# Performance work log

Measured on AMD Instinct MI355X. Metric: run time of the kernel, lower is better.

The kernel has to match this reference:

```python
import jax, jax.numpy as jnp
import numpy as np

NUM_HEADS = 8
NUM_POINTS = 4


def setup_inputs() -> dict:
    key = jax.random.key(0)
    ks = jax.random.split(key, 8)
    B, N, C, H, W = 8, 8192, 256, 128, 128
    HP2 = NUM_HEADS * NUM_POINTS * 2
    HP = NUM_HEADS * NUM_POINTS
    query = jax.random.normal(ks[0], (B, N, C), jnp.float32)
    reference_points = jax.random.uniform(ks[1], (B, N, 2), dtype=jnp.float32)
    value = jax.random.normal(ks[2], (B, C, H, W), jnp.float32)
    # learned params (offset gen is zero-init in the original; use small random
    W_off = jax.random.normal(ks[3], (C, HP2), jnp.float32) * 0.02
    b_off = jnp.zeros((HP2,), jnp.float32)
    W_attn = jax.random.normal(ks[4], (C, HP), jnp.float32) * (1.0 / np.sqrt(C))
    b_attn = jnp.zeros((HP,), jnp.float32)
    W_out = jax.random.normal(ks[5], (C, C), jnp.float32) * (1.0 / np.sqrt(C))
    b_out = jnp.zeros((C,), jnp.float32)
    return dict(query=query, reference_points=reference_points, value=value,
                W_off=W_off, b_off=b_off, W_attn=W_attn, b_attn=b_attn,
                W_out=W_out, b_out=b_out, H=H, W=W)


def reference(query, reference_points, value, W_off, b_off, W_attn, b_attn,
              W_out, b_out, H, W):
    B, N, C = query.shape
    Hh, P = NUM_HEADS, NUM_POINTS
    D = C // Hh

    offset = (query @ W_off + b_off).reshape(B, N, Hh, P, 2)
    attn = jax.nn.softmax((query @ W_attn + b_attn).reshape(B, N, Hh, P), axis=-1)

    # sampling locations in grid_sample convention: (x, y) in [-1, 1]
    ref = reference_points * 2.0 - 1.0
    loc = ref[:, :, None, None, :] + offset  # (B, N, Hh, P, 2)

    # value -> (B, Hh, H*W, D)
    val = value.reshape(B, Hh, D, H, W).transpose(0, 1, 3, 4, 2).reshape(B, Hh, H * W, D)

    # align_corners=False pixel coordinates
    x = (loc[..., 0] + 1.0) * (W * 0.5) - 0.5  # (B, N, Hh, P)
    y = (loc[..., 1] + 1.0) * (H * 0.5) - 0.5
    x0f = jnp.floor(x); y0f = jnp.floor(y)
    wx1 = x - x0f; wy1 = y - y0f
    x0 = x0f.astype(jnp.int32); y0 = y0f.astype(jnp.int32)
    x1 = x0 + 1; y1 = y0 + 1

    def gather(ix, iy, w):
        # bilinear corner gather with zero padding (mask out-of-bounds)
        valid = (ix >= 0) & (ix < W) & (iy >= 0) & (iy < H)
        idx = jnp.clip(iy, 0, H - 1) * W + jnp.clip(ix, 0, W - 1)  # (B,N,Hh,P)
        idx_t = idx.transpose(0, 2, 1, 3).reshape(B, Hh, N * P)
        g = jnp.take_along_axis(val, idx_t[..., None], axis=2)  # (B,Hh,N*P,D)
        g = g.reshape(B, Hh, N, P, D).transpose(0, 2, 1, 3, 4)  # (B,N,Hh,P,D)
        return g * (w * valid)[..., None]

    sampled = (gather(x0, y0, (1 - wx1) * (1 - wy1))
               + gather(x1, y0, wx1 * (1 - wy1))
               + gather(x0, y1, (1 - wx1) * wy1)
               + gather(x1, y1, wx1 * wy1))  # (B,N,Hh,P,D)

    out = jnp.einsum('bnhk,bnhkd->bnhd', attn, sampled).reshape(B, N, C)
    return out @ W_out + b_out
```

## Files before the change

### kernel.cpp

```cpp
#include <hip/hip_runtime.h>
#include <hip/hip_bf16.h>
#include <cstddef>

#define B_  8
#define N_  8192
#define C_  256
#define H_  128
#define W_  128
#define HH  8
#define PP  4
#define DD  32
#define HW  (H_ * W_)

typedef short bf16x8 __attribute__((ext_vector_type(8)));
typedef float f32x4  __attribute__((ext_vector_type(4)));

static __device__ __forceinline__ short f2bf_s(float f) {
    __hip_bfloat16 b = __float2bfloat16(f);
    return *reinterpret_cast<short*>(&b);
}
static __device__ __forceinline__ float bf_s2f(short s) {
    __hip_bfloat16 b = *reinterpret_cast<__hip_bfloat16*>(&s);
    return __bfloat162float(b);
}

__global__ __launch_bounds__(256) void kTP(const float* __restrict__ value,
                                           __hip_bfloat16* __restrict__ val,
                                           const float* __restrict__ W_off,
                                           const float* __restrict__ W_attn,
                                           short* __restrict__ Wc_hi,
                                           short* __restrict__ Wc_lo,
                                           const float* __restrict__ Wsrc,
                                           __hip_bfloat16* __restrict__ Wt) {
    __shared__ __align__(16) char smem[33024];
    const int t   = threadIdx.x;
    const int bid = blockIdx.x;

    if (bid < 4096) {
        float (*tile)[257] = (float (*)[257])smem;
        const int bh   = bid >> 6;
        const int pix0 = (bid & 63) * 256;
        const float* src = value + (size_t)bh * 32 * HW + pix0;
#pragma unroll
        for (int i = 0; i < 8; ++i) {
            int d  = i * 4 + (t >> 6);
            int p4 = t & 63;
            float4 v = *(const float4*)&src[(size_t)d * HW + p4 * 4];
            tile[d][p4 * 4 + 0] = v.x;
            tile[d][p4 * 4 + 1] = v.y;
            tile[d][p4 * 4 + 2] = v.z;
            tile[d][p4 * 4 + 3] = v.w;
        }
        __syncthreads();
#pragma unroll
        for (int j = 0; j < 4; ++j) {
            int pix = j * 64 + (t >> 2);
            int d0  = (t & 3) * 8;
            bf16x8 o;
#pragma unroll
            for (int k = 0; k < 8; ++k) o[k] = f2bf_s(tile[d0 + k][pix]);
            *(bf16x8*)&val[((size_t)bh * HW + pix0 + pix) * 32 + d0] = o;
        }
    } else if (bid < 4192) {
        const int c = bid - 4096;
        float v = (c < 64) ? W_off[(size_t)t * 64 + c]
                           : W_attn[(size_t)t * 32 + (c - 64)];
        short h = f2bf_s(v);
        short l = f2bf_s(v - bf_s2f(h));
        Wc_hi[(size_t)c * 256 + t] = h;
        Wc_lo[(size_t)c * 256 + t] = l;
    } else {
        float (*tile)[65] = (float (*)[65])smem;
        const int bx = bid - 4192;
        const int n0 = (bx & 3) * 64;
        const int k0 = (bx >> 2) * 64;
#pragma unroll
        for (int i = 0; i < 16; ++i) {
            int kk = i * 4 + (t >> 6);
            int nn = t & 63;
            tile[kk][nn] = Wsrc[(size_t)(k0 + kk) * 256 + n0 + nn];
        }
        __syncthreads();
#pragma unroll
        for (int i = 0; i < 16; ++i) {
            int nn = i * 4 + (t >> 6);
            int kk = t & 63;
            Wt[(size_t)(n0 + nn) * 256 + k0 + kk] = __float2bfloat16(tile[kk][nn]);
        }
    }
}

__global__ __launch_bounds__(256) void kA1M(const float* __restrict__ query,
                                            const float* __restrict__ refp,
                                            const short* __restrict__ Wc_hi,
                                            const short* __restrict__ Wc_lo,
                                            const float* __restrict__ b_off,
                                            const float* __restrict__ b_attn,
                                            float4* __restrict__ locattn) {
    __shared__ __align__(16) char smem[57344];
    short* As_hi = (short*)smem;
    short* As_lo = (short*)(smem + 16384);
    short* Bs_hi = (short*)(smem + 32768);
    short* Bs_lo = (short*)(smem + 45056);
    float* Ct    = (float*)smem;

    const int t    = threadIdx.x;
    const int lane = t & 63;
    const int w    = t >> 6;
    const int wm   = (w & 1) * 64;
    const int wn   = (w >> 1) * 48;
    const int quad = lane >> 4;
    const int l16  = lane & 15;
    const int row0 = blockIdx.x * 128;

    f32x4 acc[4][3];
#pragma unroll
    for (int mt = 0; mt < 4; ++mt)
#pragma unroll
        for (int nt = 0; nt < 3; ++nt)
            acc[mt][nt] = (f32x4){0.f, 0.f, 0.f, 0.f};

    for (int k0c = 0; k0c < 4; ++k0c) {
#pragma unroll
        for (int i = 0; i < 8; ++i) {
            int f   = t + i * 256;
            int row = f >> 4;
            int kq4 = f & 15;
            float4 q = *(const float4*)&query[(size_t)(row0 + row) * 256 +
                                              k0c * 64 + kq4 * 4];
            short4 hv, lv;
            hv.x = f2bf_s(q.x); lv.x = f2bf_s(q.x - bf_s2f(hv.x));
            hv.y = f2bf_s(q.y); lv.y = f2bf_s(q.y - bf_s2f(hv.y));
            hv.z = f2bf_s(q.z); lv.z = f2bf_s(q.z - bf_s2f(hv.z));
            hv.w = f2bf_s(q.w); lv.w = f2bf_s(q.w - bf_s2f(hv.w));
            int base = row * 64 + (((kq4 >> 1) ^ (row & 7)) * 8) + (kq4 & 1) * 4;
            *(short4*)&As_hi[base] = hv;
            *(short4*)&As_lo[base] = lv;
        }
#pragma unroll
        for (int i = 0; i < 3; ++i) {
            int idx = t + i * 256;
            int n   = idx >> 3;
            int kb  = idx & 7;
            int dst = n * 64 + ((kb ^ (n & 7)) * 8);
            *(uint4*)&Bs_hi[dst] =
                *(const uint4*)&Wc_hi[(size_t)n * 256 + k0c * 64 + kb * 8];
            *(uint4*)&Bs_lo[dst] =
                *(const uint4*)&Wc_lo[(size_t)n * 256 + k0c * 64 + kb * 8];
        }
        __syncthreads();

#pragma unroll
        for (int ks = 0; ks < 2; ++ks) {
            const int kq = ks * 4 + quad;
            bf16x8 ah[4], al[4], bh[3], bl[3];
#pragma unroll
            for (int mt = 0; mt < 4; ++mt) {
                int m = wm + mt * 16 + l16;
                ah[mt] = *(const bf16x8*)&As_hi[m * 64 + (kq ^ (m & 7)) * 8];
                al[mt] = *(const bf16x8*)&As_lo[m * 64 + (kq ^ (m & 7)) * 8];
            }
#pragma unroll
            for (int nt = 0; nt < 3; ++nt) {
                int n = wn + nt * 16 + l16;
                bh[nt] = *(const bf16x8*)&Bs_hi[n * 64 + (kq ^ (n & 7)) * 8];
                bl[nt] = *(const bf16x8*)&Bs_lo[n * 64 + (kq ^ (n & 7)) * 8];
            }
#pragma unroll
            for (int mt = 0; mt < 4; ++mt)
#pragma unroll
                for (int nt = 0; nt < 3; ++nt)
                    acc[mt][nt] = __builtin_amdgcn_mfma_f32_16x16x32_bf16(
                        ah[mt], bh[nt], acc[mt][nt], 0, 0, 0);
#pragma unroll
            for (int mt = 0; mt < 4; ++mt)
#pragma unroll
                for (int nt = 0; nt < 3; ++nt)
                    acc[mt][nt] = __builtin_amdgcn_mfma_f32_16x16x32_bf16(
                        ah[mt], bl[nt], acc[mt][nt], 0, 0, 0);
#pragma unroll
            for (int mt = 0; mt < 4; ++mt)
#pragma unroll
                for (int nt = 0; nt < 3; ++nt)
                    acc[mt][nt] = __builtin_amdgcn_mfma_f32_16x16x32_bf16(
                        al[mt], bh[nt], acc[mt][nt], 0, 0, 0);
        }
        __syncthreads();
    }

#pragma unroll
    for (int mt = 0; mt < 4; ++mt) {
#pragma unroll
        for (int nt = 0; nt < 3; ++nt) {
            int col = wn + nt * 16 + l16;
#pragma unroll
            for (int rI = 0; rI < 4; ++rI) {
                int row = wm + mt * 16 + quad * 4 + rI;
                Ct[row * 100 + col] = acc[mt][nt][rI];
            }
        }
    }
    __syncthreads();

    const int rg = t >> 3;
    const int h  = t & 7;
    float boff[8];
#pragma unroll
    for (int j = 0; j < 8; ++j) boff[j] = b_off[h * 8 + j];
    float batn[4];
#pragma unroll
    for (int j = 0; j < 4; ++j) batn[j] = b_attn[h * 4 + j];

#pragma unroll
    for (int r = 0; r < 4; ++r) {
        int row  = rg * 4 + r;
        int rowg = row0 + row;
        float rx = refp[(size_t)rowg * 2 + 0];
        float ry = refp[(size_t)rowg * 2 + 1];
        float4 lg4 = *(const float4*)&Ct[row * 100 + 64 + h * 4];
        float lg[4] = {lg4.x + batn[0], lg4.y + batn[1],
                       lg4.z + batn[2], lg4.w + batn[3]};
        float m = fmaxf(fmaxf(lg[0], lg[1]), fmaxf(lg[2], lg[3]));
        float e[4];
        float s = 0.f;
#pragma unroll
        for (int p = 0; p < 4; ++p) { e[p] = __expf(lg[p] - m); s += e[p]; }
        float inv = 1.f / s;
        float4 o0 = *(const float4*)&Ct[row * 100 + h * 8];
        float4 o1 = *(const float4*)&Ct[row * 100 + h * 8 + 4];
        float ox[4] = {o0.x + boff[0], o0.z + boff[2],
                       o1.x + boff[4], o1.z + boff[6]};
        float oy[4] = {o0.y + boff[1], o0.w + boff[3],
                       o1.y + boff[5], o1.w + boff[7]};
#pragma unroll
        for (int p = 0; p < 4; ++p) {
            float x = (rx * 2.f + ox[p]) * (W_ * 0.5f) - 0.5f;
            float y = (ry * 2.f + oy[p]) * (H_ * 0.5f) - 0.5f;
            locattn[(size_t)rowg * 32 + h * 4 + p] =
                make_float4(x, y, e[p] * inv, 0.f);
        }
    }
}

__global__ __launch_bounds__(256) void kA2(const float4* __restrict__ locattn,
                                           const __hip_bfloat16* __restrict__ val,
                                           __hip_bfloat16* __restrict__ mid) {
    __shared__ float2 ow[64][4][4];

    const int t   = threadIdx.x;
    const int bid = blockIdx.x;
    const int xcd = bid & 7;
    const int j_  = bid >> 3;
    const int bh  = xcd * 8 + (j_ >> 7);
    const int n0  = (j_ & 127) * 64;
    const int b   = bh >> 3;
    const int h   = bh & 7;

    {
        const int r = t >> 2;
        const int p = t & 3;
        float4 L = locattn[((size_t)b * N_ + n0 + r) * 32 + h * 4 + p];
        float x = L.x, y = L.y, a = L.z;
        float xf = floorf(x), yf = floorf(y);
        int x0 = (int)xf, y0 = (int)yf;
        int x1 = x0 + 1, y1 = y0 + 1;
        float wx1 = x - xf, wy1 = y - yf;
        float wx0 = 1.f - wx1, wy0 = 1.f - wy1;
        int cx0 = min(max(x0, 0), W_ - 1);
        int cx1 = min(max(x1, 0), W_ - 1);
        int cy0 = min(max(y0, 0), H_ - 1);
        int cy1 = min(max(y1, 0), H_ - 1);
        bool bx0 = (x0 >= 0) & (x0 < W_);
        bool bx1 = (x1 >= 0) & (x1 < W_);
        bool by0 = (y0 >= 0) & (y0 < H_);
        bool by1 = (y1 >= 0) & (y1 < H_);
        float w00 = a * wx0 * wy0 * ((bx0 & by0) ? 1.f : 0.f);
        float w10 = a * wx1 * wy0 * ((bx1 & by0) ? 1.f : 0.f);
        float w01 = a * wx0 * wy1 * ((bx0 & by1) ? 1.f : 0.f);
        float w11 = a * wx1 * wy1 * ((bx1 & by1) ? 1.f : 0.f);
        ow[r][p][0] = make_float2(__int_as_float(cy0 * W_ + cx0), w00);
        ow[r][p][1] = make_float2(__int_as_float(cy0 * W_ + cx1), w10);
        ow[r][p][2] = make_float2(__int_as_float(cy1 * W_ + cx0), w01);
        ow[r][p][3] = make_float2(__int_as_float(cy1 * W_ + cx1), w11);
    }
    __syncthreads();

    const int d  = t & 31;
    const int rg = t >> 5;
    const __hip_bfloat16* vb = val + (size_t)bh * HW * DD + d;
    __hip_bfloat16* mo = mid + ((size_t)b * N_ + n0) * C_ + h * DD + d;

#pragma unroll
    for (int j = 0; j < 8; ++j) {
        int r = rg * 8 + j;
        const float4* owp = (const float4*)&ow[r][0][0];
        float acc = 0.f;
#pragma unroll
        for (int p = 0; p < 4; ++p) {
            float4 u0 = owp[p * 2 + 0];
            float4 u1 = owp[p * 2 + 1];
            int o00 = __float_as_int(u0.x) * DD;
            int o10 = __float_as_int(u0.z) * DD;
            int o01 = __float_as_int(u1.x) * DD;
            int o11 = __float_as_int(u1.z) * DD;
            acc += u0.y * __bfloat162float(vb[o00]);
            acc += u0.w * __bfloat162float(vb[o10]);
            acc += u1.y * __bfloat162float(vb[o01]);
            acc += u1.w * __bfloat162float(vb[o11]);
        }
        mo[r * C_] = __float2bfloat16(acc);
    }
}

__global__ __launch_bounds__(256) void kC(const short* __restrict__ mid,
                                          const short* __restrict__ Wt,
                                          const float* __restrict__ bias,
                                          float* __restrict__ out) {
    __shared__ __align__(16) short As[128 * 64];
    __shared__ __align__(16) short Bs[128 * 64];

    const int t    = threadIdx.x;
    const int lane = t & 63;
    const int w    = t >> 6;
    const int wm   = (w & 1) * 64;
    const int wn   = (w >> 1) * 64;
    const int row0 = blockIdx.x * 128;
    const int col0 = blockIdx.y * 128;

    f32x4 acc[4][4];
#pragma unroll
    for (int mt = 0; mt < 4; ++mt)
#pragma unroll
        for (int nt = 0; nt < 4; ++nt)
            acc[mt][nt] = (f32x4){0.f, 0.f, 0.f, 0.f};

    const int sr = t >> 3;
    const int kb = t & 7;

    for (int k0 = 0; k0 < 4; ++k0) {
#pragma unroll
        for (int i = 0; i < 4; ++i) {
            int row  = sr + i * 32;
            int kbs  = (kb ^ (row & 7)) * 8;
            *(uint4*)&As[row * 64 + kbs] =
                *(const uint4*)&mid[(size_t)(row0 + row) * 256 + k0 * 64 + kb * 8];
            *(uint4*)&Bs[row * 64 + kbs] =
                *(const uint4*)&Wt[(size_t)(col0 + row) * 256 + k0 * 64 + kb * 8];
        }
        __syncthreads();

#pragma unroll
        for (int ks = 0; ks < 2; ++ks) {
            const int kq = ks * 4 + (lane >> 4);
            bf16x8 af[4], bf[4];
#pragma unroll
            for (int mt = 0; mt < 4; ++mt) {
                int m = wm + mt * 16 + (lane & 15);
                af[mt] = *(const bf16x8*)&As[m * 64 + (kq ^ (m & 7)) * 8];
            }
#pragma unroll
            for (int nt = 0; nt < 4; ++nt) {
                int n = wn + nt * 16 + (lane & 15);
                bf[nt] = *(const bf16x8*)&Bs[n * 64 + (kq ^ (n & 7)) * 8];
            }
#pragma unroll
            for (int mt = 0; mt < 4; ++mt)
#pragma unroll
                for (int nt = 0; nt < 4; ++nt)
                    acc[mt][nt] = __builtin_amdgcn_mfma_f32_16x16x32_bf16(
                        af[mt], bf[nt], acc[mt][nt], 0, 0, 0);
        }
        __syncthreads();
    }

    const int cq = lane >> 4;
#pragma unroll
    for (int nt = 0; nt < 4; ++nt) {
        int col  = col0 + wn + nt * 16 + (lane & 15);
        float bv = bias[col];
#pragma unroll
        for (int mt = 0; mt < 4; ++mt) {
#pragma unroll
            for (int rI = 0; rI < 4; ++rI) {
                int rowg = row0 + wm + mt * 16 + cq * 4 + rI;
                out[(size_t)rowg * 256 + col] = acc[mt][nt][rI] + bv;
            }
        }
    }
}

extern "C" void kernel_launch(void* const* d_in, const int* in_sizes, int n_in,
                              void* d_out, int out_size, void* d_ws, size_t ws_size,
                              hipStream_t stream) {
    const float* query  = (const float*)d_in[0];
    const float* refp   = (const float*)d_in[1];
    const float* value  = (const float*)d_in[2];
    const float* W_off  = (const float*)d_in[3];
    const float* b_off  = (const float*)d_in[4];
    const float* W_attn = (const float*)d_in[5];
    const float* b_attn = (const float*)d_in[6];
    const float* W_out  = (const float*)d_in[7];
    const float* b_out  = (const float*)d_in[8];
    float* out = (float*)d_out;

    char*           ws      = (char*)d_ws;
    __hip_bfloat16* val     = (__hip_bfloat16*)(ws);
    float4*         locattn = (float4*)(ws + 67108864);
    __hip_bfloat16* mid     = (__hip_bfloat16*)(ws + 100663296);
    __hip_bfloat16* Wt      = (__hip_bfloat16*)(ws + 134217728);
    short*          Wc_hi   = (short*)(ws + 134348800);
    short*          Wc_lo   = (short*)(ws + 134397952);

    kTP <<<dim3(4208), 256, 0, stream>>>(value, val, W_off, W_attn,
                                         Wc_hi, Wc_lo, W_out, Wt);
    kA1M<<<dim3((B_ * N_) / 128), 256, 0, stream>>>(query, refp, Wc_hi, Wc_lo,
                                                    b_off, b_attn, locattn);
    kA2 <<<dim3(B_ * HH * N_ / 64), 256, 0, stream>>>(locattn, val, mid);
    kC  <<<dim3((B_ * N_) / 128, C_ / 128), 256, 0, stream>>>(
        (const short*)mid, (const short*)Wt, b_out, out);
}
```

Before: 381.6 us.

## Fuse bilinear sampling with output projection GEMM using fp16 packed math

Merges the sampling kernel and the output-projection GEMM into one kernel. Each block builds a 64-row by 256-channel intermediate in shared memory and multiplies it by W_out with MFMA, so the mid buffer never makes a global write and read round trip. The value tensor and W_out move from bf16 to fp16, and sampling uses packed half2 FMAs with 4-channel vector gathers and compressed index/weight records. W_out tiles are register-prefetched one k-step ahead. The cost is lower accumulation precision (fp16 sums), and with 64-row blocks W_out is reloaded for every block.

```diff
diff --git a/kernel.cpp b/kernel.cpp
--- a/kernel.cpp
+++ b/kernel.cpp
@@ -1,5 +1,6 @@
 #include <hip/hip_runtime.h>
 #include <hip/hip_bf16.h>
+#include <hip/hip_fp16.h>
 #include <cstddef>
 
 #define B_  8
@@ -13,6 +14,7 @@
 #define HW  (H_ * W_)
 
 typedef short bf16x8 __attribute__((ext_vector_type(8)));
+typedef _Float16 f16x8 __attribute__((ext_vector_type(8)));
 typedef float f32x4  __attribute__((ext_vector_type(4)));
 
 static __device__ __forceinline__ short f2bf_s(float f) {
@@ -25,13 +27,13 @@
 }
 
 __global__ __launch_bounds__(256) void kTP(const float* __restrict__ value,
-                                           __hip_bfloat16* __restrict__ val,
+                                           __half* __restrict__ val,
                                            const float* __restrict__ W_off,
                                            const float* __restrict__ W_attn,
                                            short* __restrict__ Wc_hi,
                                            short* __restrict__ Wc_lo,
                                            const float* __restrict__ Wsrc,
-                                           __hip_bfloat16* __restrict__ Wt) {
+                                           __half* __restrict__ Wt) {
     __shared__ __align__(16) char smem[33024];
     const int t   = threadIdx.x;
     const int bid = blockIdx.x;
@@ -56,10 +58,14 @@
         for (int j = 0; j < 4; ++j) {
             int pix = j * 64 + (t >> 2);
             int d0  = (t & 3) * 8;
-            bf16x8 o;
-#pragma unroll
-            for (int k = 0; k < 8; ++k) o[k] = f2bf_s(tile[d0 + k][pix]);
-            *(bf16x8*)&val[((size_t)bh * HW + pix0 + pix) * 32 + d0] = o;
+            short o[8];
+#pragma unroll
+            for (int k = 0; k < 8; ++k) {
+                __half hh = __float2half(tile[d0 + k][pix]);
+                o[k] = *reinterpret_cast<short*>(&hh);
+            }
+            *(bf16x8*)&val[((size_t)bh * HW + pix0 + pix) * 32 + d0] =
+                *(bf16x8*)o;
         }
     } else if (bid < 4192) {
         const int c = bid - 4096;
@@ -85,7 +91,7 @@
         for (int i = 0; i < 16; ++i) {
             int nn = i * 4 + (t >> 6);
             int kk = t & 63;
-            Wt[(size_t)(n0 + nn) * 256 + k0 + kk] = __float2bfloat16(tile[kk][nn]);
+            Wt[(size_t)(n0 + nn) * 256 + k0 + kk] = __float2half(tile[kk][nn]);
         }
     }
 }
@@ -242,24 +248,36 @@
     }
 }
 
-__global__ __launch_bounds__(256) void kA2(const float4* __restrict__ locattn,
-                                           const __hip_bfloat16* __restrict__ val,
-                                           __hip_bfloat16* __restrict__ mid) {
-    __shared__ float2 ow[64][4][4];
-
-    const int t   = threadIdx.x;
-    const int bid = blockIdx.x;
-    const int xcd = bid & 7;
-    const int j_  = bid >> 3;
-    const int bh  = xcd * 8 + (j_ >> 7);
-    const int n0  = (j_ & 127) * 64;
-    const int b   = bh >> 3;
-    const int h   = bh & 7;
-
-    {
-        const int r = t >> 2;
-        const int p = t & 3;
-        float4 L = locattn[((size_t)b * N_ + n0 + r) * 32 + h * 4 + p];
+__global__ __launch_bounds__(256) void kAC(const float4* __restrict__ locattn,
+                                           const __half* __restrict__ val,
+                                           const __half* __restrict__ Wt,
+                                           const float* __restrict__ bias,
+                                           float* __restrict__ out) {
+    __shared__ __align__(16) char smem[65536];
+    char*  midc = smem;
+    uint4* ow   = (uint4*)(smem + 32768);
+    short* Bs   = (short*)(smem + 32768);
+
+    const int t    = threadIdx.x;
+    const int bid  = blockIdx.x;
+    const int b    = bid & 7;
+    const int n0   = (bid >> 3) * 64;
+
+    const int pn  = t >> 3;
+    const int pkb = t & 7;
+    uint4 pre[8];
+#pragma unroll
+    for (int i = 0; i < 8; ++i) {
+        int n = pn + i * 32;
+        pre[i] = *(const uint4*)&Wt[(size_t)n * 256 + pkb * 8];
+    }
+
+#pragma unroll
+    for (int i = 0; i < 8; ++i) {
+        int item = t + i * 256;
+        int r  = item >> 5;
+        int hp = item & 31;
+        float4 L = locattn[((size_t)b * N_ + n0 + r) * 32 + hp];
         float x = L.x, y = L.y, a = L.z;
         float xf = floorf(x), yf = floorf(y);
         int x0 = (int)xf, y0 = (int)yf;
@@ -274,58 +292,73 @@
         bool bx1 = (x1 >= 0) & (x1 < W_);
         bool by0 = (y0 >= 0) & (y0 < H_);
         bool by1 = (y1 >= 0) & (y1 < H_);
-        float w00 = a * wx0 * wy0 * ((bx0 & by0) ? 1.f : 0.f);
-        float w10 = a * wx1 * wy0 * ((bx1 & by0) ? 1.f : 0.f);
-        float w01 = a * wx0 * wy1 * ((bx0 & by1) ? 1.f : 0.f);
-        float w11 = a * wx1 * wy1 * ((bx1 & by1) ? 1.f : 0.f);
-        ow[r][p][0] = make_float2(__int_as_float(cy0 * W_ + cx0), w00);
-        ow[r][p][1] = make_float2(__int_as_float(cy0 * W_ + cx1), w10);
-        ow[r][p][2] = make_float2(__int_as_float(cy1 * W_ + cx0), w01);
-        ow[r][p][3] = make_float2(__int_as_float(cy1 * W_ + cx1), w11);
+        float f00 = a * wx0 * wy0 * ((bx0 & by0) ? 1.f : 0.f);
+        float f10 = a * wx1 * wy0 * ((bx1 & by0) ? 1.f : 0.f);
+        float f01 = a * wx0 * wy1 * ((bx0 & by1) ? 1.f : 0.f);
+        float f11 = a * wx1 * wy1 * ((bx1 & by1) ? 1.f : 0.f);
+        uint4 rec;
+        rec.x = (unsigned)(cy0 * W_ + cx0) | ((unsigned)(cy0 * W_ + cx1) << 16);
+        rec.y = (unsigned)(cy1 * W_ + cx0) | ((unsigned)(cy1 * W_ + cx1) << 16);
+        __half2 wA = __floats2half2_rn(f00, f10);
+        __half2 wB = __floats2half2_rn(f01, f11);
+        rec.z = *reinterpret_cast<unsigned*>(&wA);
+        rec.w = *reinterpret_cast<unsigned*>(&wB);
+        ow[item] = rec;
     }
     __syncthreads();
 
-    const int d  = t & 31;
-    const int rg = t >> 5;
-    const __hip_bfloat16* vb = val + (size_t)bh * HW * DD + d;
-    __hip_bfloat16* mo = mid + ((size_t)b * N_ + n0) * C_ + h * DD + d;
-
-#pragma unroll
-    for (int j = 0; j < 8; ++j) {
-        int r = rg * 8 + j;
-        const float4* owp = (const float4*)&ow[r][0][0];
-        float acc = 0.f;
-#pragma unroll
-        for (int p = 0; p < 4; ++p) {
-            float4 u0 = owp[p * 2 + 0];
-            float4 u1 = owp[p * 2 + 1];
-            int o00 = __float_as_int(u0.x) * DD;
-            int o10 = __float_as_int(u0.z) * DD;
-            int o01 = __float_as_int(u1.x) * DD;
-            int o11 = __float_as_int(u1.z) * DD;
-            acc += u0.y * __bfloat162float(vb[o00]);
-            acc += u0.w * __bfloat162float(vb[o10]);
-            acc += u1.y * __bfloat162float(vb[o01]);
-            acc += u1.w * __bfloat162float(vb[o11]);
-        }
-        mo[r * C_] = __float2bfloat16(acc);
-    }
-}
-
-__global__ __launch_bounds__(256) void kC(const short* __restrict__ mid,
-                                          const short* __restrict__ Wt,
-                                          const float* __restrict__ bias,
-                                          float* __restrict__ out) {
-    __shared__ __align__(16) short As[128 * 64];
-    __shared__ __align__(16) short Bs[128 * 64];
-
-    const int t    = threadIdx.x;
+    {
+        const int j8 = t & 7;
+        const int g  = t >> 3;
+        const int d8 = j8 * 4;
+#pragma unroll
+        for (int q = 0; q < 16; ++q) {
+            int pair = g * 16 + q;
+            int r = pair >> 3;
+            int h = pair & 7;
+            const char* vb = (const char*)val +
+                ((((size_t)b * 8 + h) * HW) * 32 + d8) * 2;
+            __half2 a01 = __float2half2_rn(0.f);
+            __half2 a23 = __float2half2_rn(0.f);
+#pragma unroll
+            for (int p = 0; p < 4; ++p) {
+                uint4 rec = ow[r * 32 + h * 4 + p];
+                int i0 = rec.x & 0xffff, i1 = rec.x >> 16;
+                int i2 = rec.y & 0xffff, i3 = rec.y >> 16;
+                __half2 wA = *reinterpret_cast<__half2*>(&rec.z);
+                __half2 wB = *reinterpret_cast<__half2*>(&rec.w);
+                uint2 u0 = *(const uint2*)(vb + (size_t)i0 * 64);
+                uint2 u1 = *(const uint2*)(vb + (size_t)i1 * 64);
+                uint2 u2 = *(const uint2*)(vb + (size_t)i2 * 64);
+                uint2 u3 = *(const uint2*)(vb + (size_t)i3 * 64);
+                __half2 w00 = __low2half2(wA);
+                a01 = __hfma2(*reinterpret_cast<__half2*>(&u0.x), w00, a01);
+                a23 = __hfma2(*reinterpret_cast<__half2*>(&u0.y), w00, a23);
+                __half2 w10 = __high2half2(wA);
+                a01 = __hfma2(*reinterpret_cast<__half2*>(&u1.x), w10, a01);
+                a23 = __hfma2(*reinterpret_cast<__half2*>(&u1.y), w10, a23);
+                __half2 w01 = __low2half2(wB);
+                a01 = __hfma2(*reinterpret_cast<__half2*>(&u2.x), w01, a01);
+                a23 = __hfma2(*reinterpret_cast<__half2*>(&u2.y), w01, a23);
+                __half2 w11 = __high2half2(wB);
+                a01 = __hfma2(*reinterpret_cast<__half2*>(&u3.x), w11, a01);
+                a23 = __hfma2(*reinterpret_cast<__half2*>(&u3.y), w11, a23);
+            }
+            int c8  = h * 4 + (d8 >> 3);
+            int off = r * 512 + ((c8 ^ (r & 7)) * 16) + (d8 & 7) * 2;
+            uint2 st;
+            st.x = *reinterpret_cast<unsigned*>(&a01);
+            st.y = *reinterpret_cast<unsigned*>(&a23);
+            *(uint2*)(midc + off) = st;
+        }
+    }
+    __syncthreads();
+
     const int lane = t & 63;
     const int w    = t >> 6;
-    const int wm   = (w & 1) * 64;
-    const int wn   = (w >> 1) * 64;
-    const int row0 = blockIdx.x * 128;
-    const int col0 = blockIdx.y * 128;
+    const int wn   = w * 64;
+    const int quad = lane >> 4;
+    const int l16  = lane & 15;
 
     f32x4 acc[4][4];
 #pragma unroll
@@ -334,56 +367,58 @@
         for (int nt = 0; nt < 4; ++nt)
             acc[mt][nt] = (f32x4){0.f, 0.f, 0.f, 0.f};
 
-    const int sr = t >> 3;
-    const int kb = t & 7;
-
     for (int k0 = 0; k0 < 4; ++k0) {
 #pragma unroll
-        for (int i = 0; i < 4; ++i) {
-            int row  = sr + i * 32;
-            int kbs  = (kb ^ (row & 7)) * 8;
-            *(uint4*)&As[row * 64 + kbs] =
-                *(const uint4*)&mid[(size_t)(row0 + row) * 256 + k0 * 64 + kb * 8];
-            *(uint4*)&Bs[row * 64 + kbs] =
-                *(const uint4*)&Wt[(size_t)(col0 + row) * 256 + k0 * 64 + kb * 8];
+        for (int i = 0; i < 8; ++i) {
+            int n = pn + i * 32;
+            *(uint4*)&Bs[n * 64 + ((pkb ^ (n & 7)) * 8)] = pre[i];
+        }
+        if (k0 < 3) {
+#pragma unroll
+            for (int i = 0; i < 8; ++i) {
+                int n = pn + i * 32;
+                pre[i] = *(const uint4*)&Wt[(size_t)n * 256 +
+                                            (k0 + 1) * 64 + pkb * 8];
+            }
         }
         __syncthreads();
 
 #pragma unroll
         for (int ks = 0; ks < 2; ++ks) {
-            const int kq = ks * 4 + (lane >> 4);
-            bf16x8 af[4], bf[4];
+            const int kq = ks * 4 + quad;
+            f16x8 af[4], bfv[4];
 #pragma unroll
             for (int mt = 0; mt < 4; ++mt) {
-                int m = wm + mt * 16 + (lane & 15);
-                af[mt] = *(const bf16x8*)&As[m * 64 + (kq ^ (m & 7)) * 8];
+                int m = mt * 16 + l16;
+                af[mt] = *(const f16x8*)(midc + m * 512 +
+                                         (((k0 * 8 + kq) ^ (m & 7)) * 16));
             }
 #pragma unroll
             for (int nt = 0; nt < 4; ++nt) {
-                int n = wn + nt * 16 + (lane & 15);
-                bf[nt] = *(const bf16x8*)&Bs[n * 64 + (kq ^ (n & 7)) * 8];
+                int n = wn + nt * 16 + l16;
+                bfv[nt] = *(const f16x8*)&Bs[n * 64 + ((kq ^ (n & 7)) * 8)];
             }
 #pragma unroll
             for (int mt = 0; mt < 4; ++mt)
 #pragma unroll
                 for (int nt = 0; nt < 4; ++nt)
-                    acc[mt][nt] = __builtin_amdgcn_mfma_f32_16x16x32_bf16(
-                        af[mt], bf[nt], acc[mt][nt], 0, 0, 0);
-        }
-        __syncthreads();
-    }
-
-    const int cq = lane >> 4;
+                    acc[mt][nt] = __builtin_amdgcn_mfma_f32_16x16x32_f16(
+                        af[mt], bfv[nt], acc[mt][nt], 0, 0, 0);
+        }
+        __syncthreads();
+    }
+
 #pragma unroll
     for (int nt = 0; nt < 4; ++nt) {
-        int col  = col0 + wn + nt * 16 + (lane & 15);
+        int col  = wn + nt * 16 + l16;
         float bv = bias[col];
 #pragma unroll
         for (int mt = 0; mt < 4; ++mt) {
 #pragma unroll
             for (int rI = 0; rI < 4; ++rI) {
-                int rowg = row0 + wm + mt * 16 + cq * 4 + rI;
-                out[(size_t)rowg * 256 + col] = acc[mt][nt][rI] + bv;
+                int r = mt * 16 + quad * 4 + rI;
+                out[((size_t)b * N_ + n0 + r) * 256 + col] =
+                    acc[mt][nt][rI] + bv;
             }
         }
     }
@@ -403,19 +438,17 @@
     const float* b_out  = (const float*)d_in[8];
     float* out = (float*)d_out;
 
-    char*           ws      = (char*)d_ws;
-    __hip_bfloat16* val     = (__hip_bfloat16*)(ws);
-    float4*         locattn = (float4*)(ws + 67108864);
-    __hip_bfloat16* mid     = (__hip_bfloat16*)(ws + 100663296);
-    __hip_bfloat16* Wt      = (__hip_bfloat16*)(ws + 134217728);
-    short*          Wc_hi   = (short*)(ws + 134348800);
-    short*          Wc_lo   = (short*)(ws + 134397952);
+    char*   ws      = (char*)d_ws;
+    __half* val     = (__half*)(ws);
+    float4* locattn = (float4*)(ws + 67108864);
+    __half* Wt      = (__half*)(ws + 134217728);
+    short*  Wc_hi   = (short*)(ws + 134348800);
+    short*  Wc_lo   = (short*)(ws + 134397952);
 
     kTP <<<dim3(4208), 256, 0, stream>>>(value, val, W_off, W_attn,
                                          Wc_hi, Wc_lo, W_out, Wt);
     kA1M<<<dim3((B_ * N_) / 128), 256, 0, stream>>>(query, refp, Wc_hi, Wc_lo,
                                                     b_off, b_attn, locattn);
-    kA2 <<<dim3(B_ * HH * N_ / 64), 256, 0, stream>>>(locattn, val, mid);
-    kC  <<<dim3((B_ * N_) / 128, C_ / 128), 256, 0, stream>>>(
-        (const short*)mid, (const short*)Wt, b_out, out);
-}
+    kAC <<<dim3((B_ * N_) / 64), 256, 0, stream>>>(locattn, val, Wt,
+                                                   b_out, out);
+}
```

New measurement: 405.5 us. 6.3% more time.
